# Optimization experiments

Hardware: AMD Instinct MI355X
Metric: run time of the kernel (lower is better)

The kernel has to match this reference:

```python
import jax, jax.numpy as jnp
import numpy as np


def _affine_mats(thetas, lambda1s, lambda2s, H, W):
    # Replicates torch.stack(rows, dim=1) then stack(dim=2): the 'rows' end up as COLUMNS,
    # exactly matching the original module's construction.
    z = jnp.zeros_like(lambda1s)
    o = jnp.ones_like(lambda1s)
    scale = jnp.stack([jnp.stack([lambda1s, z, z], 1),
                       jnp.stack([z, lambda2s, z], 1),
                       jnp.stack([z, z, o], 1)], axis=2)  # [B,3,3]
    th = -thetas
    rot = jnp.stack([jnp.stack([jnp.cos(th), jnp.sin(th), z], 1),
                     jnp.stack([-jnp.sin(th), jnp.cos(th), z], 1),
                     jnp.stack([z, z, o], 1)], axis=2)
    trans = jnp.stack([jnp.stack([o, z, o * W], 1),
                       jnp.stack([z, o, o * H], 1),
                       jnp.stack([z, z, o], 1)], axis=2)
    fw = rot @ trans                       # forward_warp
    fws = scale @ fw                       # forward_warp_scaled
    overall = jnp.linalg.inv(jnp.linalg.inv(fw) @ fws)
    return overall[:, 0:2, :]              # [B,2,3]


def _affine_grid(theta, H, W):
    # torch affine_grid, align_corners=False: normalized pixel-center coords in [-1,1]
    xs = (jnp.arange(W, dtype=theta.dtype) + 0.5) * (2.0 / W) - 1.0
    ys = (jnp.arange(H, dtype=theta.dtype) + 0.5) * (2.0 / H) - 1.0
    X, Y = jnp.meshgrid(xs, ys)                        # [H,W]
    base = jnp.stack([X, Y, jnp.ones_like(X)], -1)     # [H,W,3]
    return jnp.einsum('bij,hwj->bhwi', theta, base)    # [B,H,W,2] (x,y)


def _grid_sample_bilinear_zeros(x, grid):
    # torch grid_sample(mode='bilinear', padding_mode='zeros', align_corners=False)
    B, C, H, W = x.shape
    gx = (grid[..., 0] + 1.0) * (W * 0.5) - 0.5        # [B,H,W] source pixel coords
    gy = (grid[..., 1] + 1.0) * (H * 0.5) - 0.5
    x0 = jnp.floor(gx); y0 = jnp.floor(gy)
    x1 = x0 + 1.0;      y1 = y0 + 1.0
    wx1 = gx - x0; wx0 = 1.0 - wx1
    wy1 = gy - y0; wy0 = 1.0 - wy1
    x0i = x0.astype(jnp.int32); x1i = x1.astype(jnp.int32)
    y0i = y0.astype(jnp.int32); y1i = y1.astype(jnp.int32)
    b_idx = jnp.arange(B)[:, None, None]

    def gather(yi, xi):
        yc = jnp.clip(yi, 0, H - 1)
        xc = jnp.clip(xi, 0, W - 1)
        v = x[b_idx, :, yc, xc]                        # [B,H,W,C]
        m = ((yi >= 0) & (yi < H) & (xi >= 0) & (xi < W)).astype(x.dtype)
        return v * m[..., None]

    out = (gather(y0i, x0i) * (wy0 * wx0)[..., None]
           + gather(y0i, x1i) * (wy0 * wx1)[..., None]
           + gather(y1i, x0i) * (wy1 * wx0)[..., None]
           + gather(y1i, x1i) * (wy1 * wx1)[..., None])  # [B,H,W,C]
    return jnp.transpose(out, (0, 3, 1, 2))            # [B,C,H,W]


def setup_inputs() -> dict:
    key = jax.random.key(0)
    k1, k2, k3, k4 = jax.random.split(key, 4)
    B, C, H, W = 32, 3, 512, 512
    return {
        'x': jax.random.normal(k1, (B, C, H, W), dtype=jnp.float32),
        'thetas': jax.random.normal(k2, (B,), dtype=jnp.float32),
        'lambda1s': jax.random.uniform(k3, (B,), dtype=jnp.float32),
        'lambda2s': jax.random.uniform(k4, (B,), dtype=jnp.float32),
    }


def reference(x, thetas, lambda1s, lambda2s):
    H, W = x.shape[2], x.shape[3]
    theta = _affine_mats(thetas, lambda1s, lambda2s, H, W)   # [B,2,3]
    grid = _affine_grid(theta, H, W)                         # [B,H,W,2]
    return _grid_sample_bilinear_zeros(x, grid).astype(jnp.float32)
```

## Files before the change

kernel.cpp:

```cpp
#include <hip/hip_runtime.h>
#include <math.h>

constexpr int B = 32;
constexpr int C = 3;
constexpr int H = 512;
constexpr int W = 512;
constexpr int HW = H * W;

__global__ __launch_bounds__(256)
void warp_kernel(const float* __restrict__ x,
                 const float* __restrict__ thetas,
                 const float* __restrict__ l1s,
                 const float* __restrict__ l2s,
                 float* __restrict__ out) {
    const int b = blockIdx.y;

    __shared__ float sc[4];
    if (threadIdx.x == 0) {
        double th = -(double)thetas[b];
        double c = cos(th), s = sin(th);
        double a = 1.0 / (double)l1s[b];
        double d = 1.0 / (double)l2s[b];
        sc[0] = (float)(a * c * c + d * s * s);
        sc[1] = (float)(c * s * (d - a));
        sc[2] = sc[1];
        sc[3] = (float)(a * s * s + d * c * c);
    }
    __syncthreads();
    const float t00 = sc[0], t01 = sc[1], t10 = sc[2], t11 = sc[3];

    const int tid   = threadIdx.x;
    const int lane  = tid & 63;
    const int wv    = tid >> 6;
    const int h     = (blockIdx.x << 1) | (wv >> 1);
    const int wbase = (wv & 1) << 8;

    const float Y = ((float)h + 0.5f) * (2.0f / (float)H) - 1.0f;

    int   off0[4], off1[4];
    float sw0[4], sw1[4], sw2[4], sw3[4];
    bool  any_valid = false;

    #pragma unroll
    for (int j = 0; j < 4; ++j) {
        const int w = wbase + (j << 6) + lane;
        const float X = ((float)w + 0.5f) * (2.0f / (float)W) - 1.0f;
        const float gx = (t00 * X + t01 * Y + 1.0f) * ((float)W * 0.5f) - 0.5f;
        const float gy = (t10 * X + t11 * Y + 1.0f) * ((float)H * 0.5f) - 0.5f;

        const float x0f = floorf(gx), y0f = floorf(gy);
        const float wx1 = gx - x0f, wx0 = 1.0f - wx1;
        const float wy1 = gy - y0f, wy0 = 1.0f - wy1;

        const int x0 = (int)x0f, y0 = (int)y0f;
        const int x1 = x0 + 1,  y1 = y0 + 1;

        const bool vx0 = ((unsigned)x0 < (unsigned)W);
        const bool vx1 = ((unsigned)x1 < (unsigned)W);
        const bool vy0 = ((unsigned)y0 < (unsigned)H);
        const bool vy1 = ((unsigned)y1 < (unsigned)H);
        any_valid = any_valid || ((vy0 || vy1) && (vx0 || vx1));

        const int xb  = min(max(x0, 0), W - 2);
        const bool xeq = (x0 == xb);
        off0[j] = min(max(y0, 0), H - 1) * W + xb;
        off1[j] = min(max(y1, 0), H - 1) * W + xb;

        const float m00 = (vy0 && vx0) ? 1.0f : 0.0f;
        const float m01 = (vy0 && vx1) ? 1.0f : 0.0f;
        const float m10 = (vy1 && vx0) ? 1.0f : 0.0f;
        const float m11 = (vy1 && vx1) ? 1.0f : 0.0f;
        const float w00 = wy0 * wx0 * m00, w01 = wy0 * wx1 * m01;
        const float w10 = wy1 * wx0 * m10, w11 = wy1 * wx1 * m11;

        sw0[j] = xeq ? w00 : w01;
        sw1[j] = xeq ? w01 : w00;
        sw2[j] = xeq ? w10 : w11;
        sw3[j] = xeq ? w11 : w10;
    }

    float r[C][4];
    #pragma unroll
    for (int ch = 0; ch < C; ++ch)
        #pragma unroll
        for (int j = 0; j < 4; ++j) r[ch][j] = 0.0f;

    if (__any(any_valid)) {
        const float* __restrict__ base = x + (size_t)b * C * HW;
        float2 v0[4][C], v1[4][C];
        #pragma unroll
        for (int j = 0; j < 4; ++j) {
            #pragma unroll
            for (int ch = 0; ch < C; ++ch) {
                const float* __restrict__ p = base + ch * HW;
                v0[j][ch] = *reinterpret_cast<const float2*>(p + off0[j]);
                v1[j][ch] = *reinterpret_cast<const float2*>(p + off1[j]);
            }
        }
        #pragma unroll
        for (int j = 0; j < 4; ++j) {
            #pragma unroll
            for (int ch = 0; ch < C; ++ch) {
                r[ch][j] = v0[j][ch].x * sw0[j] + v0[j][ch].y * sw1[j]
                         + v1[j][ch].x * sw2[j] + v1[j][ch].y * sw3[j];
            }
        }
    }

    const size_t obase = (size_t)b * C * HW + (size_t)h * W + (size_t)wbase + lane;
    #pragma unroll
    for (int ch = 0; ch < C; ++ch) {
        #pragma unroll
        for (int j = 0; j < 4; ++j) {
            __builtin_nontemporal_store(r[ch][j], out + obase + (size_t)ch * HW + (j << 6));
        }
    }
}

extern "C" void kernel_launch(void* const* d_in, const int* in_sizes, int n_in,
                              void* d_out, int out_size, void* d_ws, size_t ws_size,
                              hipStream_t stream) {
    const float* x      = (const float*)d_in[0];
    const float* thetas = (const float*)d_in[1];
    const float* l1s    = (const float*)d_in[2];
    const float* l2s    = (const float*)d_in[3];
    float* out          = (float*)d_out;

    warp_kernel<<<dim3(H / 2, B), 256, 0, stream>>>(x, thetas, l1s, l2s, out);
}
```

Baseline: 206.7 us.

## Use bounds-checked buffer loads to skip out-of-range samples per lane

Replaces global float2 gathers with AMD raw buffer loads bound to one per-channel resource. Out-of-range rows and columns get an offset the hardware bounds check rejects and returns zero for, so the wave-level __any early-out is dropped and invalid lanes fetch no memory. It also sets a minimum of 4 blocks per CU in the launch bounds and replaces the nontemporal output stores with plain stores. The risk is that fully invalid waves now issue load instructions they used to skip, and plain stores may pollute the cache.

```diff
diff --git a/kernel.cpp b/kernel.cpp
--- a/kernel.cpp
+++ b/kernel.cpp
@@ -7,7 +7,15 @@
 constexpr int W = 512;
 constexpr int HW = H * W;
 
-__global__ __launch_bounds__(256)
+typedef unsigned int v2u __attribute__((ext_vector_type(2)));
+typedef float        v2f __attribute__((ext_vector_type(2)));
+
+static __device__ __forceinline__ v2f bload2(__amdgpu_buffer_rsrc_t r, int voff) {
+    v2u u = __builtin_amdgcn_raw_buffer_load_b64(r, voff, 0, 0);
+    return __builtin_bit_cast(v2f, u);
+}
+
+__global__ __launch_bounds__(256, 4)
 void warp_kernel(const float* __restrict__ x,
                  const float* __restrict__ thetas,
                  const float* __restrict__ l1s,
@@ -37,9 +45,15 @@
 
     const float Y = ((float)h + 0.5f) * (2.0f / (float)H) - 1.0f;
 
-    int   off0[4], off1[4];
+    __amdgpu_buffer_rsrc_t rs[C];
+    #pragma unroll
+    for (int ch = 0; ch < C; ++ch) {
+        rs[ch] = __builtin_amdgcn_make_buffer_rsrc(
+            (void*)(x + (size_t)(b * C + ch) * HW), (short)0, HW * 4, 0x00020000);
+    }
+
+    int   voff0[4], voff1[4];
     float sw0[4], sw1[4], sw2[4], sw3[4];
-    bool  any_valid = false;
 
     #pragma unroll
     for (int j = 0; j < 4; ++j) {
@@ -59,12 +73,15 @@
         const bool vx1 = ((unsigned)x1 < (unsigned)W);
         const bool vy0 = ((unsigned)y0 < (unsigned)H);
         const bool vy1 = ((unsigned)y1 < (unsigned)H);
-        any_valid = any_valid || ((vy0 || vy1) && (vx0 || vx1));
+        const bool anyx = vx0 || vx1;
 
-        const int xb  = min(max(x0, 0), W - 2);
+        const int xb   = min(max(x0, 0), W - 2);
         const bool xeq = (x0 == xb);
-        off0[j] = min(max(y0, 0), H - 1) * W + xb;
-        off1[j] = min(max(y1, 0), H - 1) * W + xb;
+
+        const int yc0 = min(max(y0, -1), H);
+        const int yc1 = min(max(y1, -1), H);
+        voff0[j] = anyx ? (yc0 * W + xb) * 4 : -1;
+        voff1[j] = anyx ? (yc1 * W + xb) * 4 : -1;
 
         const float m00 = (vy0 && vx0) ? 1.0f : 0.0f;
         const float m01 = (vy0 && vx1) ? 1.0f : 0.0f;
@@ -79,31 +96,23 @@
         sw3[j] = xeq ? w11 : w10;
     }
 
+    v2f v0[4][C], v1[4][C];
+    #pragma unroll
+    for (int j = 0; j < 4; ++j) {
+        #pragma unroll
+        for (int ch = 0; ch < C; ++ch) {
+            v0[j][ch] = bload2(rs[ch], voff0[j]);
+            v1[j][ch] = bload2(rs[ch], voff1[j]);
+        }
+    }
+
     float r[C][4];
     #pragma unroll
-    for (int ch = 0; ch < C; ++ch)
+    for (int j = 0; j < 4; ++j) {
         #pragma unroll
-        for (int j = 0; j < 4; ++j) r[ch][j] = 0.0f;
-
-    if (__any(any_valid)) {
-        const float* __restrict__ base = x + (size_t)b * C * HW;
-        float2 v0[4][C], v1[4][C];
-        #pragma unroll
-        for (int j = 0; j < 4; ++j) {
-            #pragma unroll
-            for (int ch = 0; ch < C; ++ch) {
-                const float* __restrict__ p = base + ch * HW;
-                v0[j][ch] = *reinterpret_cast<const float2*>(p + off0[j]);
-                v1[j][ch] = *reinterpret_cast<const float2*>(p + off1[j]);
-            }
-        }
-        #pragma unroll
-        for (int j = 0; j < 4; ++j) {
-            #pragma unroll
-            for (int ch = 0; ch < C; ++ch) {
-                r[ch][j] = v0[j][ch].x * sw0[j] + v0[j][ch].y * sw1[j]
-                         + v1[j][ch].x * sw2[j] + v1[j][ch].y * sw3[j];
-            }
+        for (int ch = 0; ch < C; ++ch) {
+            r[ch][j] = v0[j][ch].x * sw0[j] + v0[j][ch].y * sw1[j]
+                     + v1[j][ch].x * sw2[j] + v1[j][ch].y * sw3[j];
         }
     }
 
@@ -112,7 +121,7 @@
     for (int ch = 0; ch < C; ++ch) {
         #pragma unroll
         for (int j = 0; j < 4; ++j) {
-            __builtin_nontemporal_store(r[ch][j], out + obase + (size_t)ch * HW + (j << 6));
+            out[obase + (size_t)ch * HW + (j << 6)] = r[ch][j];
         }
     }
 }
```

Result: faster. 197.1 us (-4.6%).
